# Kernel optimization log

Hardware: AMD Instinct MI355X
Metric: run time of the kernel (lower is better)

Reference implementation:

```python
import jax, jax.numpy as jnp
import numpy as np

H = 1024        # hidden_size
V = 50257       # output_size (vocab)
L = 2048        # number of encoder annotations


def setup_inputs() -> dict:
    key = jax.random.key(0)
    ks = jax.random.split(key, 24)
    s = 0.02
    inp = {
        "input_tok": jax.random.randint(ks[0], (1,), 0, V),
        "hidden": jax.random.normal(ks[1], (1, H), jnp.float32),
        "encoder_outputs": jax.random.normal(ks[2], (L, 1, 2 * H), jnp.float32),
        "cell_state": jax.random.normal(ks[3], (1, H), jnp.float32),
        # embedding: Linear(V, H)
        "W_emb": jax.random.normal(ks[4], (V, H), jnp.float32) * s,
        "b_emb": jnp.zeros((H,), jnp.float32),
        # attn_layer: Linear(3H, H); attn_output: Linear(H, 1)
        "W_attn": jax.random.normal(ks[5], (3 * H, H), jnp.float32) * s,
        "b_attn": jnp.zeros((H,), jnp.float32),
        "W_attn_out": jax.random.normal(ks[6], (H, 1), jnp.float32) * s,
        "b_attn_out": jnp.zeros((1,), jnp.float32),
        # LSTM gates: Linear(3H + H, H) each
        "W_i": jax.random.normal(ks[7], (4 * H, H), jnp.float32) * s,
        "b_i": jnp.zeros((H,), jnp.float32),
        "W_o": jax.random.normal(ks[8], (4 * H, H), jnp.float32) * s,
        "b_o": jnp.zeros((H,), jnp.float32),
        "W_f": jax.random.normal(ks[9], (4 * H, H), jnp.float32) * s,
        "b_f": jnp.zeros((H,), jnp.float32),
        "W_c": jax.random.normal(ks[10], (4 * H, H), jnp.float32) * s,
        "b_c": jnp.zeros((H,), jnp.float32),
        # output_layer: Linear(4H, V)
        "W_out": jax.random.normal(ks[11], (4 * H, V), jnp.float32) * s,
        "b_out": jnp.zeros((V,), jnp.float32),
    }
    return inp


def reference(input_tok, hidden, encoder_outputs, cell_state,
              W_emb, b_emb, W_attn, b_attn, W_attn_out, b_attn_out,
              W_i, b_i, W_o, b_o, W_f, b_f, W_c, b_c, W_out, b_out):
    # embedding of one-hot previous token: [1, V] @ [V, H] -> [1, H]
    one_hot = jax.nn.one_hot(input_tok, V, dtype=W_emb.dtype)
    emb = one_hot @ W_emb + b_emb                     # [1, H]
    # dropout_p = 0.0 -> identity (eval-mode reference)

    enc = encoder_outputs[:, 0, :]                    # [L, 2H]
    hid_b = jnp.broadcast_to(hidden, (enc.shape[0], hidden.shape[1]))
    attn_in = jnp.concatenate([enc, hid_b], axis=1)   # [L, 3H]
    scores = jnp.tanh(attn_in @ W_attn + b_attn) @ W_attn_out + b_attn_out  # [L, 1]
    # exp(e_ij) / sum_j exp(e_ij)  ==  softmax over encoder steps
    attn_weights = jax.nn.softmax(scores, axis=0)     # [L, 1]
    context = jnp.sum(attn_weights * enc, axis=0, keepdims=True)  # [1, 2H]

    # LSTM step on cat(embedding, context) with state (hidden, cell_state)
    lstm_in = jnp.concatenate([emb, context], axis=1)              # [1, 3H]
    combined = jnp.concatenate([lstm_in, hidden], axis=1)          # [1, 4H]
    i_g = jax.nn.sigmoid(combined @ W_i + b_i)
    o_g = jax.nn.sigmoid(combined @ W_o + b_o)
    f_g = jax.nn.sigmoid(combined @ W_f + b_f)
    c_g = jnp.tanh(combined @ W_c + b_c)
    new_cell = f_g * cell_state + i_g * c_g
    next_hidden = o_g * jnp.tanh(new_cell)

    out = jnp.concatenate([emb, hidden, context], axis=1) @ W_out + b_out  # [1, V]
    log_softmax = jax.nn.log_softmax(out, axis=1)
    return (log_softmax, next_hidden, attn_weights, new_cell)
```

## Files before the change

### kernel.cpp

```cpp
#include <hip/hip_runtime.h>
#include <hip/hip_bf16.h>
#include <math.h>

#define Hh 1024
#define Vv 50257
#define Ll 2048
#define H2 2048
#define H4 4096

#define WS_EMB  0
#define WS_CTX  3072
#define WS_LOG  9216
#define WS_PAIR 59474
#define OA_BYTES 245760u
#define OB_BYTES 8634368u
#define PP 50264
#define WS_PART_F 3210240
#define WS_HBP 4014464
#define WS_SCP 4080000
#define WS_GATEP 4112768

#define OUT_NH Vv
#define OUT_AW (Vv + 1024)
#define OUT_NC (Vv + 3072)

typedef __attribute__((ext_vector_type(8))) short bf16x8;
typedef __attribute__((ext_vector_type(4))) float f32x4;
typedef __attribute__((ext_vector_type(4), aligned(4))) float f32x4u;

__device__ __forceinline__ float sigmoidf_(float x) { return 1.f / (1.f + expf(-x)); }
__device__ __forceinline__ unsigned short f2bf(float f) {
    union { float f; unsigned u; } v; v.f = f;
    unsigned r = v.u + 0x7FFF + ((v.u >> 16) & 1);
    return (unsigned short)(r >> 16);
}

__device__ __forceinline__ void stream_wout(const float* __restrict__ W_out,
        const float* __restrict__ xs, int k0, int v4, float* __restrict__ part_row) {
    if (v4 + 3 < Vv) {
        const char* p = (const char*)(W_out + (size_t)k0 * Vv + v4);
        const size_t st = (size_t)Vv * 4;
        f32x4 a0 = (f32x4){0.f,0.f,0.f,0.f}, a1 = a0, a2 = a0, a3 = a0;
        f32x4 a4 = a0, a5 = a0, a6 = a0, a7 = a0;
        for (int i = 0; i < 256; i += 8) {
            f32x4u w0 = __builtin_nontemporal_load((const f32x4u*)(p));
            f32x4u w1 = __builtin_nontemporal_load((const f32x4u*)(p + st));
            f32x4u w2 = __builtin_nontemporal_load((const f32x4u*)(p + 2 * st));
            f32x4u w3 = __builtin_nontemporal_load((const f32x4u*)(p + 3 * st));
            f32x4u w4 = __builtin_nontemporal_load((const f32x4u*)(p + 4 * st));
            f32x4u w5 = __builtin_nontemporal_load((const f32x4u*)(p + 5 * st));
            f32x4u w6 = __builtin_nontemporal_load((const f32x4u*)(p + 6 * st));
            f32x4u w7 = __builtin_nontemporal_load((const f32x4u*)(p + 7 * st));
            a0 += w0 * xs[i];     a1 += w1 * xs[i + 1];
            a2 += w2 * xs[i + 2]; a3 += w3 * xs[i + 3];
            a4 += w4 * xs[i + 4]; a5 += w5 * xs[i + 5];
            a6 += w6 * xs[i + 6]; a7 += w7 * xs[i + 7];
            p += 8 * st;
        }
        f32x4 a = ((a0 + a1) + (a2 + a3)) + ((a4 + a5) + (a6 + a7));
        __builtin_nontemporal_store(a, (f32x4u*)(part_row + v4));
    } else if (v4 < Vv) {
        for (int jj = 0; jj < 4 && v4 + jj < Vv; ++jj) {
            const float* p = W_out + (size_t)k0 * Vv + v4 + jj;
            float a = 0.f;
            for (int i = 0; i < 256; ++i) { a += xs[i] * (*p); p += Vv; }
            part_row[v4 + jj] = a;
        }
    }
}

__global__ __launch_bounds__(256) void kPrep(const int* __restrict__ tok,
        const float* __restrict__ W_emb, const float* __restrict__ b_emb,
        const float* __restrict__ enc, const float* __restrict__ W_attn,
        const float* __restrict__ hidden, float* __restrict__ ws, char* __restrict__ wsb) {
    __shared__ union { float a[16][132]; float b[32][68]; } sh;
    int bx = blockIdx.x, t = threadIdx.x;
    if (bx < 2048) {
        int mt = bx >> 4, kc = bx & 15;
        {
            int row = t >> 4, c8 = (t & 15) * 8;
            const float* src = enc + (size_t)(mt * 16 + row) * H2 + kc * 128 + c8;
            float4 v0 = *(const float4*)src;
            float4 v1 = *(const float4*)(src + 4);
            *(float4*)&sh.a[row][c8] = v0;
            *(float4*)&sh.a[row][c8 + 4] = v1;
        }
        __syncthreads();
        int ktl = t >> 6, l = t & 63;
        int r2 = l & 15, k8 = (l >> 4) * 8;
        bf16x8 o;
#pragma unroll
        for (int j = 0; j < 8; ++j) o[j] = (short)f2bf(sh.a[r2][ktl * 32 + k8 + j]);
        *(bf16x8*)(wsb + OA_BYTES + ((size_t)(mt * 64 + kc * 4 + ktl)) * 1024 + l * 16) = o;
    } else if (bx < 3072) {
        int bxx = bx - 2048;
        int kt = bxx >> 4, nc = bxx & 15;
        {
            int r = t >> 3, c8 = (t & 7) * 8;
            const float* src = W_attn + (size_t)(kt * 32 + r) * Hh + nc * 64 + c8;
            float4 v0 = *(const float4*)src;
            float4 v1 = *(const float4*)(src + 4);
            *(float4*)&sh.b[r][c8] = v0;
            *(float4*)&sh.b[r][c8 + 4] = v1;
        }
        __syncthreads();
        int ntl = t >> 6, l = t & 63;
        int col = ntl * 16 + (l & 15), k8 = (l >> 4) * 8;
        bf16x8 o;
#pragma unroll
        for (int j = 0; j < 8; ++j) o[j] = (short)f2bf(sh.b[k8 + j][col]);
        *(bf16x8*)(wsb + OB_BYTES + ((size_t)((nc * 4 + ntl) * 64 + kt)) * 1024 + l * 16) = o;
    } else if (bx < 3328) {
        int bxx = bx - 3072;
        int hc = bxx & 3, kc = bxx >> 2;
        int h = hc * 256 + t;
        int k0 = kc * 16;
        const float* p = W_attn + (size_t)(H2 + k0) * Hh + h;
        float acc = 0.f;
#pragma unroll
        for (int k = 0; k < 16; ++k) { acc += hidden[k0 + k] * __builtin_nontemporal_load(p); p += Hh; }
        ws[WS_HBP + kc * 1024 + h] = acc;
    } else {
        int i = (bx - 3328) * 256 + t;
        if (i < 1024) ws[WS_EMB + i] = W_emb[(size_t)tok[0] * Hh + i] + b_emb[i];
        else          ws[WS_CTX + (i - 1024)] = 0.f;
    }
}

__global__ __launch_bounds__(128, 1) void kG(const char* __restrict__ wsb,
        const float* __restrict__ b_attn, const float* __restrict__ Wo,
        float* __restrict__ ws) {
    __shared__ float hbv[64];
    int bx = blockIdx.x, t = threadIdx.x;
    int bm = bx >> 4, bn = bx & 15;
    int w = t >> 6, l = t & 63;
    if (t < 64) {
        int n = bn * 64 + t;
        float a = b_attn[n];
#pragma unroll 16
        for (int kc = 0; kc < 64; ++kc) a += ws[WS_HBP + kc * 1024 + n];
        hbv[t] = a;
    }
    __syncthreads();
    int mt0 = bm * 4 + w * 2;
    int nt0 = bn * 4;
    const char* pa0 = wsb + OA_BYTES + (size_t)(mt0)     * 65536 + l * 16;
    const char* pa1 = wsb + OA_BYTES + (size_t)(mt0 + 1) * 65536 + l * 16;
    const char* pb0 = wsb + OB_BYTES + (size_t)(nt0)     * 65536 + l * 16;
    const char* pb1 = wsb + OB_BYTES + (size_t)(nt0 + 1) * 65536 + l * 16;
    const char* pb2 = wsb + OB_BYTES + (size_t)(nt0 + 2) * 65536 + l * 16;
    const char* pb3 = wsb + OB_BYTES + (size_t)(nt0 + 3) * 65536 + l * 16;

    f32x4 acc[2][4];
#pragma unroll
    for (int i = 0; i < 2; ++i)
#pragma unroll
        for (int j = 0; j < 4; ++j) acc[i][j] = (f32x4){0.f, 0.f, 0.f, 0.f};

    bf16x8 As[8][2], Bs[8][4];
#define LOADK(s, kk) { int o_ = (kk) * 1024; \
    As[s][0] = *(const bf16x8*)(pa0 + o_); As[s][1] = *(const bf16x8*)(pa1 + o_); \
    Bs[s][0] = *(const bf16x8*)(pb0 + o_); Bs[s][1] = *(const bf16x8*)(pb1 + o_); \
    Bs[s][2] = *(const bf16x8*)(pb2 + o_); Bs[s][3] = *(const bf16x8*)(pb3 + o_); }
#define MFMAK(s) { \
    _Pragma("unroll") for (int mr = 0; mr < 2; ++mr) \
    _Pragma("unroll") for (int nr = 0; nr < 4; ++nr) \
        acc[mr][nr] = __builtin_amdgcn_mfma_f32_16x16x32_bf16(As[s][mr], Bs[s][nr], acc[mr][nr], 0, 0, 0); }

    LOADK(0, 0) LOADK(1, 1) LOADK(2, 2) LOADK(3, 3)
    LOADK(4, 4) LOADK(5, 5) LOADK(6, 6) LOADK(7, 7)
    for (int kt = 0; kt < 56; kt += 8) {
        MFMAK(0) LOADK(0, kt + 8)
        MFMAK(1) LOADK(1, kt + 9)
        MFMAK(2) LOADK(2, kt + 10)
        MFMAK(3) LOADK(3, kt + 11)
        MFMAK(4) LOADK(4, kt + 12)
        MFMAK(5) LOADK(5, kt + 13)
        MFMAK(6) LOADK(6, kt + 14)
        MFMAK(7) LOADK(7, kt + 15)
    }
    MFMAK(0) MFMAK(1) MFMAK(2) MFMAK(3) MFMAK(4) MFMAK(5) MFMAK(6) MFMAK(7)
#undef LOADK
#undef MFMAK

    float sp[8];
#pragma unroll
    for (int i = 0; i < 8; ++i) sp[i] = 0.f;
    int nl = l & 15;
#pragma unroll
    for (int nr = 0; nr < 4; ++nr) {
        float hb = hbv[nr * 16 + nl];
        float wo = Wo[bn * 64 + nr * 16 + nl];
#pragma unroll
        for (int mr = 0; mr < 2; ++mr)
#pragma unroll
            for (int r = 0; r < 4; ++r)
                sp[mr * 4 + r] += tanhf(acc[mr][nr][r] + hb) * wo;
    }
#pragma unroll
    for (int m = 1; m <= 8; m <<= 1)
#pragma unroll
        for (int i = 0; i < 8; ++i) sp[i] += __shfl_xor(sp[i], m, 64);
    if ((l & 15) == 0) {
        int mbase = bm * 64 + w * 32 + (l >> 4) * 4;
#pragma unroll
        for (int mr = 0; mr < 2; ++mr)
#pragma unroll
            for (int r = 0; r < 4; ++r)
                ws[WS_SCP + bn * 2048 + mbase + mr * 16 + r] = sp[mr * 4 + r];
    }
}

__global__ __launch_bounds__(256) void k34(const float* __restrict__ enc,
        float* __restrict__ ws, float* __restrict__ out) {
    __shared__ float red[256];
    __shared__ float wl[64];
    int bx = blockIdx.x, t = threadIdx.x;
    int jc = bx & 7, lc = bx >> 3;
    float s[8];
    float mx = -INFINITY;
#pragma unroll
    for (int i = 0; i < 8; ++i) {
        int m = i * 256 + t;
        float v = 0.f;
#pragma unroll
        for (int bn = 0; bn < 16; ++bn) v += ws[WS_SCP + bn * 2048 + m];
        s[i] = v;
        mx = fmaxf(mx, v);
    }
    red[t] = mx;
    __syncthreads();
    for (int off = 128; off > 0; off >>= 1) {
        if (t < off) red[t] = fmaxf(red[t], red[t + off]);
        __syncthreads();
    }
    float M = red[0];
    __syncthreads();
    float se = 0.f;
#pragma unroll
    for (int i = 0; i < 8; ++i) se += expf(s[i] - M);
    red[t] = se;
    __syncthreads();
    for (int off = 128; off > 0; off >>= 1) {
        if (t < off) red[t] += red[t + off];
        __syncthreads();
    }
    float invZ = 1.f / red[0];
    int l0 = lc * 64;
    if (t < 64) {
        int m = l0 + t;
        float v = 0.f;
#pragma unroll
        for (int bn = 0; bn < 16; ++bn) v += ws[WS_SCP + bn * 2048 + m];
        wl[t] = expf(v - M) * invZ;
    }
    __syncthreads();
    if (jc == 0 && t < 64) out[OUT_AW + l0 + t] = wl[t];
    int j = jc * 256 + t;
    float acc = 0.f;
#pragma unroll 8
    for (int i = 0; i < 64; ++i)
        acc += wl[i] * enc[(size_t)(l0 + i) * H2 + j];
    atomicAdd(&ws[WS_CTX + j], acc);
}

__global__ __launch_bounds__(256) void kS(const float* __restrict__ W_out,
        const float* __restrict__ W_i, const float* __restrict__ W_o,
        const float* __restrict__ W_f, const float* __restrict__ W_c,
        const float* __restrict__ hidden, float* __restrict__ ws) {
    __shared__ float xs[256];
    int bx = blockIdx.x, t = threadIdx.x;
    if (bx < 128) {
        int g = bx & 3, kc = bx >> 2;
        int k0 = kc * 128;
        const float* Wm = (g == 0) ? W_i : (g == 1) ? W_o : (g == 2) ? W_f : W_c;
        const f32x4* p = (const f32x4*)(Wm + (size_t)k0 * Hh) + t;
        f32x4 a = (f32x4){0.f, 0.f, 0.f, 0.f};
#pragma unroll 8
        for (int k = k0; k < k0 + 128; ++k) {
            float x = (k < 1024) ? ws[WS_EMB + k] : (k < 3072) ? ws[WS_CTX + (k - 1024)] : hidden[k - 3072];
            f32x4 wv = __builtin_nontemporal_load(p);
            a += wv * x;
            p += 256;
        }
        *(f32x4*)&ws[WS_GATEP + (size_t)(g * 32 + kc) * 1024 + t * 4] = a;
    } else {
        int s = bx - 128;
        int kc = s / 50, vb = s % 50;
        int k0 = kc * 256;
        {
            int k = k0 + t;
            xs[t] = (k < 1024) ? ws[WS_EMB + k] : (k < 2048) ? hidden[k - 1024] : ws[WS_CTX + (k - 2048)];
        }
        __syncthreads();
        stream_wout(W_out, xs, k0, vb * 1024 + t * 4, ws + WS_PART_F + (size_t)kc * PP);
    }
}

__global__ __launch_bounds__(256) void kF(const float* __restrict__ b_i,
        const float* __restrict__ b_o, const float* __restrict__ b_f,
        const float* __restrict__ b_c, const float* __restrict__ cell,
        const float* __restrict__ b_out, float* __restrict__ ws, float* __restrict__ out) {
    int bx = blockIdx.x, t = threadIdx.x;
    if (bx < 197) {
        __shared__ float sm[256];
        int v = bx * 256 + t;
        float x = -INFINITY;
        if (v < Vv) {
            x = b_out[v];
            const float* pp = ws + WS_PART_F + v;
#pragma unroll
            for (int kc = 0; kc < 16; ++kc) x += pp[(size_t)kc * PP];
            ws[WS_LOG + v] = x;
        }
        sm[t] = x;
        __syncthreads();
        for (int off = 128; off > 0; off >>= 1) {
            if (t < off) sm[t] = fmaxf(sm[t], sm[t + off]);
            __syncthreads();
        }
        float m = sm[0];
        __syncthreads();
        sm[t] = (v < Vv) ? expf(x - m) : 0.f;
        __syncthreads();
        for (int off = 128; off > 0; off >>= 1) {
            if (t < off) sm[t] += sm[t + off];
            __syncthreads();
        }
        if (t == 0) { ws[WS_PAIR + 2 * bx] = m; ws[WS_PAIR + 2 * bx + 1] = sm[0]; }
    } else {
#pragma unroll
        for (int r = 0; r < 4; ++r) {
            int h = t + r * 256;
            float gp[4];
#pragma unroll
            for (int g = 0; g < 4; ++g) {
                float s = 0.f;
#pragma unroll 8
                for (int kc = 0; kc < 32; ++kc)
                    s += ws[WS_GATEP + (size_t)(g * 32 + kc) * 1024 + h];
                gp[g] = s;
            }
            float ig = sigmoidf_(gp[0] + b_i[h]);
            float og = sigmoidf_(gp[1] + b_o[h]);
            float fg = sigmoidf_(gp[2] + b_f[h]);
            float cg = tanhf(gp[3] + b_c[h]);
            float nc = fg * cell[h] + ig * cg;
            out[OUT_NC + h] = nc;
            out[OUT_NH + h] = og * tanhf(nc);
        }
    }
}

__global__ __launch_bounds__(256) void k8bc(const float* __restrict__ ws, float* __restrict__ out) {
    __shared__ float sm[256], ss[256];
    int t = threadIdx.x;
    float m = (t < 197) ? ws[WS_PAIR + 2 * t] : -INFINITY;
    float s = (t < 197) ? ws[WS_PAIR + 2 * t + 1] : 0.f;
    sm[t] = m;
    __syncthreads();
    for (int off = 128; off > 0; off >>= 1) {
        if (t < off) sm[t] = fmaxf(sm[t], sm[t + off]);
        __syncthreads();
    }
    float M = sm[0];
    ss[t] = s * expf(m - M);
    __syncthreads();
    for (int off = 128; off > 0; off >>= 1) {
        if (t < off) ss[t] += ss[t + off];
        __syncthreads();
    }
    float logZ = M + logf(ss[0]);
    int v = blockIdx.x * 256 + t;
    if (v < Vv) out[v] = ws[WS_LOG + v] - logZ;
}

extern "C" void kernel_launch(void* const* d_in, const int* in_sizes, int n_in,
                              void* d_out, int out_size, void* d_ws, size_t ws_size,
                              hipStream_t stream) {
    const int*   tok        = (const int*)d_in[0];
    const float* hidden     = (const float*)d_in[1];
    const float* enc        = (const float*)d_in[2];
    const float* cell       = (const float*)d_in[3];
    const float* W_emb      = (const float*)d_in[4];
    const float* b_emb      = (const float*)d_in[5];
    const float* W_attn     = (const float*)d_in[6];
    const float* b_attn     = (const float*)d_in[7];
    const float* W_attn_out = (const float*)d_in[8];
    const float* W_i   = (const float*)d_in[10];
    const float* b_i   = (const float*)d_in[11];
    const float* W_o   = (const float*)d_in[12];
    const float* b_o   = (const float*)d_in[13];
    const float* W_f   = (const float*)d_in[14];
    const float* b_f   = (const float*)d_in[15];
    const float* W_c   = (const float*)d_in[16];
    const float* b_c   = (const float*)d_in[17];
    const float* W_out = (const float*)d_in[18];
    const float* b_out = (const float*)d_in[19];
    float* out = (float*)d_out;
    float* ws  = (float*)d_ws;
    char*  wsb = (char*)d_ws;

    kPrep<<<dim3(3340), dim3(256), 0, stream>>>(tok, W_emb, b_emb, enc, W_attn, hidden, ws, wsb);
    kG<<<dim3(512), dim3(128), 0, stream>>>(wsb, b_attn, W_attn_out, ws);
    k34<<<dim3(256), dim3(256), 0, stream>>>(enc, ws, out);
    kS<<<dim3(928), dim3(256), 0, stream>>>(W_out, W_i, W_o, W_f, W_c, hidden, ws);
    kF<<<dim3(198), dim3(256), 0, stream>>>(b_i, b_o, b_f, b_c, cell, b_out, ws, out);
    k8bc<<<dim3(197), dim3(256), 0, stream>>>(ws, out);
}
```

Measured before the change: 231.0 us.

## Fuse six decoder kernels into one cooperative persistent kernel with grid syncs

Replaces the six-launch pipeline with a single cooperative kernel of 512 blocks that uses grid-wide syncs between stages. The emb/hidden part of the W_out stream now runs alongside the attention prep work instead of after it. Launch gaps and inter-kernel drains go away, and bandwidth-heavy streaming overlaps with compute-light stages. In exchange, the grid is limited to co-resident blocks, grid.sync adds its own overhead, and the attention GEMM is re-tiled with smaller per-wave tiles. The old path is kept as a fallback if the cooperative launch fails.

After: 522.6 us. +126.2%, slower.

```diff
diff --git a/kernel.cpp b/kernel.cpp
--- a/kernel.cpp
+++ b/kernel.cpp
@@ -1,6 +1,9 @@
 #include <hip/hip_runtime.h>
+#include <hip/hip_cooperative_groups.h>
 #include <hip/hip_bf16.h>
 #include <math.h>
+
+namespace cg = cooperative_groups;
 
 #define Hh 1024
 #define Vv 50257
@@ -69,6 +72,298 @@
     }
 }
 
+__global__ __launch_bounds__(256, 2) void coopK(
+        const int* __restrict__ tok, const float* __restrict__ hidden,
+        const float* __restrict__ enc, const float* __restrict__ cell,
+        const float* __restrict__ W_emb, const float* __restrict__ b_emb,
+        const float* __restrict__ W_attn, const float* __restrict__ b_attn,
+        const float* __restrict__ Wao,
+        const float* __restrict__ Wgi, const float* __restrict__ bgi,
+        const float* __restrict__ Wgo, const float* __restrict__ bgo,
+        const float* __restrict__ Wgf, const float* __restrict__ bgf,
+        const float* __restrict__ Wgc, const float* __restrict__ bgc,
+        const float* __restrict__ W_out, const float* __restrict__ b_out,
+        float* __restrict__ out, float* __restrict__ ws, char* __restrict__ wsb) {
+    cg::grid_group gg = cg::this_grid();
+    __shared__ float s1[2176];
+    int bx = blockIdx.x, t = threadIdx.x;
+
+    if (bx < 400) {
+        int kc = bx / 50, vb = bx % 50;
+        int k0 = kc * 256;
+        int k = k0 + t;
+        s1[t] = (k < 1024) ? (W_emb[(size_t)tok[0] * Hh + k] + b_emb[k]) : hidden[k - 1024];
+        __syncthreads();
+        stream_wout(W_out, s1, k0, vb * 1024 + t * 4, ws + WS_PART_F + (size_t)kc * PP);
+    } else {
+        for (int u = bx - 400; u < 3340; u += 112) {
+            __syncthreads();
+            if (u < 2048) {
+                int mt = u >> 4, kc = u & 15;
+                float (*a)[132] = (float(*)[132])s1;
+                int row = t >> 4, c8 = (t & 15) * 8;
+                const float* src = enc + (size_t)(mt * 16 + row) * H2 + kc * 128 + c8;
+                float4 v0 = *(const float4*)src;
+                float4 v1 = *(const float4*)(src + 4);
+                *(float4*)&a[row][c8] = v0;
+                *(float4*)&a[row][c8 + 4] = v1;
+                __syncthreads();
+                int ktl = t >> 6, l = t & 63;
+                int r2 = l & 15, k8 = (l >> 4) * 8;
+                bf16x8 o;
+#pragma unroll
+                for (int j = 0; j < 8; ++j) o[j] = (short)f2bf(a[r2][ktl * 32 + k8 + j]);
+                *(bf16x8*)(wsb + OA_BYTES + ((size_t)(mt * 64 + kc * 4 + ktl)) * 1024 + l * 16) = o;
+            } else if (u < 3072) {
+                int uu = u - 2048;
+                int kt = uu >> 4, nc = uu & 15;
+                float (*b)[68] = (float(*)[68])s1;
+                int r = t >> 3, c8 = (t & 7) * 8;
+                const float* src = W_attn + (size_t)(kt * 32 + r) * Hh + nc * 64 + c8;
+                float4 v0 = *(const float4*)src;
+                float4 v1 = *(const float4*)(src + 4);
+                *(float4*)&b[r][c8] = v0;
+                *(float4*)&b[r][c8 + 4] = v1;
+                __syncthreads();
+                int ntl = t >> 6, l = t & 63;
+                int col = ntl * 16 + (l & 15), k8 = (l >> 4) * 8;
+                bf16x8 o;
+#pragma unroll
+                for (int j = 0; j < 8; ++j) o[j] = (short)f2bf(b[k8 + j][col]);
+                *(bf16x8*)(wsb + OB_BYTES + ((size_t)((nc * 4 + ntl) * 64 + kt)) * 1024 + l * 16) = o;
+            } else if (u < 3328) {
+                int uu = u - 3072;
+                int hc = uu & 3, kc = uu >> 2;
+                int h = hc * 256 + t;
+                int k0 = kc * 16;
+                const float* p = W_attn + (size_t)(H2 + k0) * Hh + h;
+                float acc = 0.f;
+#pragma unroll
+                for (int k = 0; k < 16; ++k) { acc += hidden[k0 + k] * __builtin_nontemporal_load(p); p += Hh; }
+                ws[WS_HBP + kc * 1024 + h] = acc;
+            } else {
+                int i = (u - 3328) * 256 + t;
+                if (i < 1024) ws[WS_EMB + i] = W_emb[(size_t)tok[0] * Hh + i] + b_emb[i];
+                else          ws[WS_CTX + (i - 1024)] = 0.f;
+            }
+        }
+    }
+    gg.sync();
+
+    {
+        int bm = bx >> 4, bn = bx & 15;
+        int w = t >> 6, l = t & 63;
+        if (t < 64) {
+            int n = bn * 64 + t;
+            float a = b_attn[n];
+#pragma unroll 16
+            for (int kc = 0; kc < 64; ++kc) a += ws[WS_HBP + kc * 1024 + n];
+            s1[t] = a;
+        }
+        __syncthreads();
+        int mt0 = bm * 4 + w;
+        int nt0 = bn * 4;
+        const char* pa  = wsb + OA_BYTES + (size_t)mt0 * 65536 + l * 16;
+        const char* pb0 = wsb + OB_BYTES + (size_t)(nt0)     * 65536 + l * 16;
+        const char* pb1 = wsb + OB_BYTES + (size_t)(nt0 + 1) * 65536 + l * 16;
+        const char* pb2 = wsb + OB_BYTES + (size_t)(nt0 + 2) * 65536 + l * 16;
+        const char* pb3 = wsb + OB_BYTES + (size_t)(nt0 + 3) * 65536 + l * 16;
+
+        f32x4 acc[4];
+#pragma unroll
+        for (int j = 0; j < 4; ++j) acc[j] = (f32x4){0.f, 0.f, 0.f, 0.f};
+        bf16x8 As[4], Bs[4][4];
+#define LOADK(s, kk) { int o_ = (kk) * 1024; \
+    As[s] = *(const bf16x8*)(pa + o_); \
+    Bs[s][0] = *(const bf16x8*)(pb0 + o_); Bs[s][1] = *(const bf16x8*)(pb1 + o_); \
+    Bs[s][2] = *(const bf16x8*)(pb2 + o_); Bs[s][3] = *(const bf16x8*)(pb3 + o_); }
+#define MFMAK(s) { \
+    _Pragma("unroll") for (int nr = 0; nr < 4; ++nr) \
+        acc[nr] = __builtin_amdgcn_mfma_f32_16x16x32_bf16(As[s], Bs[s][nr], acc[nr], 0, 0, 0); }
+        LOADK(0, 0) LOADK(1, 1) LOADK(2, 2) LOADK(3, 3)
+        for (int kt = 0; kt < 60; kt += 4) {
+            MFMAK(0) LOADK(0, kt + 4)
+            MFMAK(1) LOADK(1, kt + 5)
+            MFMAK(2) LOADK(2, kt + 6)
+            MFMAK(3) LOADK(3, kt + 7)
+        }
+        MFMAK(0) MFMAK(1) MFMAK(2) MFMAK(3)
+#undef LOADK
+#undef MFMAK
+        float sp[4] = {0.f, 0.f, 0.f, 0.f};
+        int nl = l & 15;
+#pragma unroll
+        for (int nr = 0; nr < 4; ++nr) {
+            float hb = s1[nr * 16 + nl];
+            float wo = Wao[bn * 64 + nr * 16 + nl];
+#pragma unroll
+            for (int r = 0; r < 4; ++r)
+                sp[r] += tanhf(acc[nr][r] + hb) * wo;
+        }
+#pragma unroll
+        for (int m = 1; m <= 8; m <<= 1)
+#pragma unroll
+            for (int r = 0; r < 4; ++r) sp[r] += __shfl_xor(sp[r], m, 64);
+        if (nl == 0) {
+            int mbase = bm * 64 + w * 16 + (l >> 4) * 4;
+#pragma unroll
+            for (int r = 0; r < 4; ++r)
+                ws[WS_SCP + bn * 2048 + mbase + r] = sp[r];
+        }
+    }
+    gg.sync();
+
+    if (bx < 256) {
+        float* red = s1;
+        float* wl  = s1 + 256;
+        int jc = bx & 7, lc = bx >> 3;
+        float s[8];
+        float mx = -INFINITY;
+#pragma unroll
+        for (int i = 0; i < 8; ++i) {
+            int m = i * 256 + t;
+            float v = 0.f;
+#pragma unroll
+            for (int bn = 0; bn < 16; ++bn) v += ws[WS_SCP + bn * 2048 + m];
+            s[i] = v;
+            mx = fmaxf(mx, v);
+        }
+        red[t] = mx;
+        __syncthreads();
+        for (int off = 128; off > 0; off >>= 1) {
+            if (t < off) red[t] = fmaxf(red[t], red[t + off]);
+            __syncthreads();
+        }
+        float M = red[0];
+        __syncthreads();
+        float se = 0.f;
+#pragma unroll
+        for (int i = 0; i < 8; ++i) se += expf(s[i] - M);
+        red[t] = se;
+        __syncthreads();
+        for (int off = 128; off > 0; off >>= 1) {
+            if (t < off) red[t] += red[t + off];
+            __syncthreads();
+        }
+        float invZ = 1.f / red[0];
+        int l0 = lc * 64;
+        if (t < 64) {
+            int m = l0 + t;
+            float v = 0.f;
+#pragma unroll
+            for (int bn = 0; bn < 16; ++bn) v += ws[WS_SCP + bn * 2048 + m];
+            wl[t] = expf(v - M) * invZ;
+        }
+        __syncthreads();
+        if (jc == 0 && t < 64) out[OUT_AW + l0 + t] = wl[t];
+        int j = jc * 256 + t;
+        float acc = 0.f;
+#pragma unroll 8
+        for (int i = 0; i < 64; ++i)
+            acc += wl[i] * enc[(size_t)(l0 + i) * H2 + j];
+        atomicAdd(&ws[WS_CTX + j], acc);
+    }
+    gg.sync();
+
+    if (bx < 400) {
+        int kc = 8 + bx / 50, vb = bx % 50;
+        int k0 = kc * 256;
+        s1[t] = ws[WS_CTX + k0 - 2048 + t];
+        __syncthreads();
+        stream_wout(W_out, s1, k0, vb * 1024 + t * 4, ws + WS_PART_F + (size_t)kc * PP);
+    } else {
+        for (int u = bx - 400; u < 128; u += 112) {
+            int g = u & 3, kc = u >> 2;
+            int k0 = kc * 128;
+            const float* Wm = (g == 0) ? Wgi : (g == 1) ? Wgo : (g == 2) ? Wgf : Wgc;
+            const f32x4* p = (const f32x4*)(Wm + (size_t)k0 * Hh) + t;
+            f32x4 a = (f32x4){0.f, 0.f, 0.f, 0.f};
+#pragma unroll 8
+            for (int k = k0; k < k0 + 128; ++k) {
+                float x = (k < 1024) ? ws[WS_EMB + k] : (k < 3072) ? ws[WS_CTX + (k - 1024)] : hidden[k - 3072];
+                f32x4 wv = __builtin_nontemporal_load(p);
+                a += wv * x;
+                p += 256;
+            }
+            *(f32x4*)&ws[WS_GATEP + (size_t)(g * 32 + kc) * 1024 + t * 4] = a;
+        }
+    }
+    gg.sync();
+
+    if (bx < 197) {
+        float* sm = s1;
+        int v = bx * 256 + t;
+        float x = -INFINITY;
+        if (v < Vv) {
+            x = b_out[v];
+            const float* pp = ws + WS_PART_F + v;
+#pragma unroll
+            for (int kc = 0; kc < 16; ++kc) x += pp[(size_t)kc * PP];
+            ws[WS_LOG + v] = x;
+        }
+        sm[t] = x;
+        __syncthreads();
+        for (int off = 128; off > 0; off >>= 1) {
+            if (t < off) sm[t] = fmaxf(sm[t], sm[t + off]);
+            __syncthreads();
+        }
+        float m = sm[0];
+        __syncthreads();
+        sm[t] = (v < Vv) ? expf(x - m) : 0.f;
+        __syncthreads();
+        for (int off = 128; off > 0; off >>= 1) {
+            if (t < off) sm[t] += sm[t + off];
+            __syncthreads();
+        }
+        if (t == 0) { ws[WS_PAIR + 2 * bx] = m; ws[WS_PAIR + 2 * bx + 1] = sm[0]; }
+    } else if (bx == 197) {
+#pragma unroll
+        for (int r = 0; r < 4; ++r) {
+            int h = t + r * 256;
+            float gp[4];
+#pragma unroll
+            for (int g = 0; g < 4; ++g) {
+                float s = 0.f;
+#pragma unroll 8
+                for (int kc = 0; kc < 32; ++kc)
+                    s += ws[WS_GATEP + (size_t)(g * 32 + kc) * 1024 + h];
+                gp[g] = s;
+            }
+            float ig = sigmoidf_(gp[0] + bgi[h]);
+            float og = sigmoidf_(gp[1] + bgo[h]);
+            float fg = sigmoidf_(gp[2] + bgf[h]);
+            float cg = tanhf(gp[3] + bgc[h]);
+            float nc = fg * cell[h] + ig * cg;
+            out[OUT_NC + h] = nc;
+            out[OUT_NH + h] = og * tanhf(nc);
+        }
+    }
+    gg.sync();
+
+    if (bx < 197) {
+        float* sm = s1;
+        float* ss = s1 + 256;
+        float m = (t < 197) ? ws[WS_PAIR + 2 * t] : -INFINITY;
+        float s = (t < 197) ? ws[WS_PAIR + 2 * t + 1] : 0.f;
+        sm[t] = m;
+        __syncthreads();
+        for (int off = 128; off > 0; off >>= 1) {
+            if (t < off) sm[t] = fmaxf(sm[t], sm[t + off]);
+            __syncthreads();
+        }
+        float M = sm[0];
+        ss[t] = s * expf(m - M);
+        __syncthreads();
+        for (int off = 128; off > 0; off >>= 1) {
+            if (t < off) ss[t] += ss[t + off];
+            __syncthreads();
+        }
+        float logZ = M + logf(ss[0]);
+        int v = bx * 256 + t;
+        if (v < Vv) out[v] = ws[WS_LOG + v] - logZ;
+    }
+}
+
 __global__ __launch_bounds__(256) void kPrep(const int* __restrict__ tok,
         const float* __restrict__ W_emb, const float* __restrict__ b_emb,
         const float* __restrict__ enc, const float* __restrict__ W_attn,
@@ -150,13 +445,11 @@
     const char* pb1 = wsb + OB_BYTES + (size_t)(nt0 + 1) * 65536 + l * 16;
     const char* pb2 = wsb + OB_BYTES + (size_t)(nt0 + 2) * 65536 + l * 16;
     const char* pb3 = wsb + OB_BYTES + (size_t)(nt0 + 3) * 65536 + l * 16;
-
     f32x4 acc[2][4];
 #pragma unroll
     for (int i = 0; i < 2; ++i)
 #pragma unroll
         for (int j = 0; j < 4; ++j) acc[i][j] = (f32x4){0.f, 0.f, 0.f, 0.f};
-
     bf16x8 As[8][2], Bs[8][4];
 #define LOADK(s, kk) { int o_ = (kk) * 1024; \
     As[s][0] = *(const bf16x8*)(pa0 + o_); As[s][1] = *(const bf16x8*)(pa1 + o_); \
@@ -166,7 +459,6 @@
     _Pragma("unroll") for (int mr = 0; mr < 2; ++mr) \
     _Pragma("unroll") for (int nr = 0; nr < 4; ++nr) \
         acc[mr][nr] = __builtin_amdgcn_mfma_f32_16x16x32_bf16(As[s][mr], Bs[s][nr], acc[mr][nr], 0, 0, 0); }
-
     LOADK(0, 0) LOADK(1, 1) LOADK(2, 2) LOADK(3, 3)
     LOADK(4, 4) LOADK(5, 5) LOADK(6, 6) LOADK(7, 7)
     for (int kt = 0; kt < 56; kt += 8) {
@@ -182,7 +474,6 @@
     MFMAK(0) MFMAK(1) MFMAK(2) MFMAK(3) MFMAK(4) MFMAK(5) MFMAK(6) MFMAK(7)
 #undef LOADK
 #undef MFMAK
-
     float sp[8];
 #pragma unroll
     for (int i = 0; i < 8; ++i) sp[i] = 0.f;
@@ -401,10 +692,28 @@
     float* ws  = (float*)d_ws;
     char*  wsb = (char*)d_ws;
 
-    kPrep<<<dim3(3340), dim3(256), 0, stream>>>(tok, W_emb, b_emb, enc, W_attn, hidden, ws, wsb);
-    kG<<<dim3(512), dim3(128), 0, stream>>>(wsb, b_attn, W_attn_out, ws);
-    k34<<<dim3(256), dim3(256), 0, stream>>>(enc, ws, out);
-    kS<<<dim3(928), dim3(256), 0, stream>>>(W_out, W_i, W_o, W_f, W_c, hidden, ws);
-    kF<<<dim3(198), dim3(256), 0, stream>>>(b_i, b_o, b_f, b_c, cell, b_out, ws, out);
-    k8bc<<<dim3(197), dim3(256), 0, stream>>>(ws, out);
-}
+    int dev = 0, coop = 0;
+    hipGetDevice(&dev);
+    hipDeviceGetAttribute(&coop, hipDeviceAttributeCooperativeLaunch, dev);
+
+    hipError_t err = hipErrorUnknown;
+    if (coop) {
+        void* args[] = {
+            (void*)&tok, (void*)&hidden, (void*)&enc, (void*)&cell,
+            (void*)&W_emb, (void*)&b_emb, (void*)&W_attn, (void*)&b_attn,
+            (void*)&W_attn_out,
+            (void*)&W_i, (void*)&b_i, (void*)&W_o, (void*)&b_o,
+            (void*)&W_f, (void*)&b_f, (void*)&W_c, (void*)&b_c,
+            (void*)&W_out, (void*)&b_out, (void*)&out, (void*)&ws, (void*)&wsb };
+        err = hipLaunchCooperativeKernel((const void*)coopK, dim3(512), dim3(256),
+                                         args, 0, stream);
+    }
+    if (err != hipSuccess) {
+        kPrep<<<dim3(3340), dim3(256), 0, stream>>>(tok, W_emb, b_emb, enc, W_attn, hidden, ws, wsb);
+        kG<<<dim3(512), dim3(128), 0, stream>>>(wsb, b_attn, W_attn_out, ws);
+        k34<<<dim3(256), dim3(256), 0, stream>>>(enc, ws, out);
+        kS<<<dim3(928), dim3(256), 0, stream>>>(W_out, W_i, W_o, W_f, W_c, hidden, ws);
+        kF<<<dim3(198), dim3(256), 0, stream>>>(b_i, b_o, b_f, b_c, cell, b_out, ws, out);
+        k8bc<<<dim3(197), dim3(256), 0, stream>>>(ws, out);
+    }
+}
```
